# Optimization experiments

Measured on AMD Instinct MI355X. Metric: run time of the kernel, lower is better.

The kernel has to match this reference:

```python
import jax, jax.numpy as jnp
import numpy as np
import math

QUERY_LEN = 64
VALUES_LEN = 64
NUM_HEADS = 16


def setup_inputs() -> dict:
    key = jax.random.key(0)
    k1, k2, k3, k4 = jax.random.split(key, 4)
    B, G, N = 2, 4, 1024
    D = QUERY_LEN * NUM_HEADS  # 1024
    queries = jax.random.normal(k1, (B, G, N, D), dtype=jnp.float32)
    keys = jax.random.normal(k2, (B, G, N, D), dtype=jnp.float32)
    values = jax.random.normal(k3, (B, G, N, VALUES_LEN * NUM_HEADS), dtype=jnp.float32)
    neuron_bank_connectivity_sub = jax.random.uniform(k4, (1, G, 1, N, N), dtype=jnp.float32)
    return {
        "queries": queries,
        "keys": keys,
        "values": values,
        "neuron_bank_connectivity_sub": neuron_bank_connectivity_sub,
    }


def reference(queries, keys, values, neuron_bank_connectivity_sub):
    B, G, N, _ = queries.shape
    H, dq, dv = NUM_HEADS, QUERY_LEN, VALUES_LEN
    # view last dim as (vec_len, num_heads), move heads forward: [B,G,H,N,d]
    q = queries.reshape(B, G, N, dq, H).transpose(0, 1, 4, 2, 3)
    k = keys.reshape(B, G, N, dq, H).transpose(0, 1, 4, 2, 3)
    v = values.reshape(B, G, N, dv, H).transpose(0, 1, 4, 2, 3)
    scores = jnp.einsum('bghnd,bghmd->bghnm', q, k) / math.sqrt(dq)
    probs = jax.nn.softmax(scores - neuron_bank_connectivity_sub, axis=-1)
    out = jnp.einsum('bghnm,bghmd->bghnd', probs, v)  # [B,G,H,N,dv]
    # Faithful to original: view() applied to the contiguous [B,G,H,N,dv] buffer
    return out.reshape(B, G, N, H * dv)
```

## Files before the change

### kernel.cpp

```cpp
#include <hip/hip_runtime.h>
#include <hip/hip_bf16.h>
#include <math.h>

#define B_ 2
#define G_ 4
#define N_ 1024
#define H_ 16
#define D_ 64
#define BG_ (B_*G_)
#define BGH_ (B_*G_*H_)
#define MK 64
#define LOG2E 1.44269504f
#define QSCALE (0.125f * LOG2E)

typedef __bf16 bf16;
typedef bf16 bf16x8 __attribute__((ext_vector_type(8)));
typedef bf16 bf16x2 __attribute__((ext_vector_type(2)));
typedef float f32x4 __attribute__((ext_vector_type(4)));
typedef float f32x16 __attribute__((ext_vector_type(16)));
typedef int i32x4 __attribute__((ext_vector_type(4)));
typedef unsigned u32x2 __attribute__((ext_vector_type(2)));

static __device__ __forceinline__ f32x16 mfma32(bf16x8 a, bf16x8 b, f32x16 c) {
    return __builtin_amdgcn_mfma_f32_32x32x16_bf16(a, b, c, 0, 0, 0);
}

static __device__ __forceinline__ unsigned pk2(float a, float b) {
    bf16x2 t; t[0] = (bf16)a; t[1] = (bf16)b;
    return __builtin_bit_cast(unsigned, t);
}

static __device__ __forceinline__ void pl32swap(unsigned& a, unsigned& b, int hi) {
#if __has_builtin(__builtin_amdgcn_permlane32_swap)
    u32x2 r = __builtin_amdgcn_permlane32_swap(a, b, false, false);
    a = r[0]; b = r[1];
    (void)hi;
#else
    unsigned ax = (unsigned)__shfl_xor((int)a, 32, 64);
    unsigned bx = (unsigned)__shfl_xor((int)b, 32, 64);
    unsigned na = hi ? bx : a;
    unsigned nb = hi ? b : ax;
    a = na; b = nb;
#endif
}

static __device__ __forceinline__ void gll16(const void* gsrc, void* ldst, int lane) {
#if __has_builtin(__builtin_amdgcn_global_load_lds)
    (void)lane;
    __builtin_amdgcn_global_load_lds((const __attribute__((address_space(1))) void*)gsrc,
                                     (__attribute__((address_space(3))) void*)ldst, 16, 0, 0);
#else
    *(bf16x8*)((bf16*)ldst + lane * 8) = *(const bf16x8*)((const bf16*)gsrc);
#endif
}

#define HS 1160
#define NS 72

__global__ __launch_bounds__(256) void transpose_fused(
    const float* __restrict__ q, const float* __restrict__ k, const float* __restrict__ v,
    const float* __restrict__ bias,
    bf16* __restrict__ qt, bf16* __restrict__ ktb, bf16* __restrict__ vtT16,
    float* __restrict__ biasX)
{
    __shared__ __attribute__((aligned(16))) bf16 lds[16 * HS];
    int bx = blockIdx.x;
    int t = threadIdx.x;

    if (bx >= 3 * 512) {
        int idx = bx - 3 * 512;
        int gg  = idx >> 8;
        int tl  = idx & 255;
        int q0  = (tl >> 4) * 64;
        int m0  = (tl & 15) * 64;
        float* ldsF = (float*)lds;

        int mi = t & 15, qr = t >> 4;
#pragma unroll
        for (int rr = 0; rr < 4; ++rr) {
            int row = qr + rr * 16;
            f32x4 val = *(const f32x4*)(bias + ((size_t)(gg * N_ + q0 + row) * N_ + m0 + 4 * mi));
            *(f32x4*)(&ldsF[row * 68 + 4 * mi]) = val;
        }
        __syncthreads();
        int qr2 = t & 63, mb0 = t >> 6;
#pragma unroll
        for (int kk = 0; kk < 4; ++kk) {
            int mbi = mb0 + kk * 4;
            f32x4 vv = *(const f32x4*)(&ldsF[qr2 * 68 + 4 * mbi]);
            *(f32x4*)(biasX + (((size_t)gg * 256 + m0 / 4 + mbi) * N_ + q0 + qr2) * 4) = vv;
        }
        return;
    }

    int tensor = bx >> 9;
    int rr = bx & 511;
    int bg = rr >> 6;
    int tile = rr & 63;
    int n0 = tile * 16;

    const float* src = (tensor == 0) ? q : (tensor == 1) ? k : v;
    float scale = (tensor == 0) ? QSCALE : 1.0f;
    const float* sb = src + (size_t)bg * N_ * 1024 + (size_t)n0 * 1024;

    int h0 = 4 * (t & 3);
    int d  = t >> 2;
    int wbase = h0 * HS + d;
#pragma unroll 4
    for (int i = 0; i < 16; ++i) {
        float4 val = ((const float4*)(sb + (size_t)i * 1024))[t];
        bf16* p = &lds[wbase + i * NS];
        p[0]        = (bf16)(val.x * scale);
        p[HS]       = (bf16)(val.y * scale);
        p[2 * HS]   = (bf16)(val.z * scale);
        p[3 * HS]   = (bf16)(val.w * scale);
    }
    __syncthreads();

    if (tensor < 2) {
        bf16* dst = (tensor == 0) ? qt : ktb;
        int n  = (t >> 3) & 15;
        int db = t & 7;
        int hb = t >> 7;
#pragma unroll
        for (int i = 0; i < 8; ++i) {
            int h = 2 * i + hb;
            bf16x8 vv = *(const bf16x8*)(&lds[h * HS + n * NS + db * 8]);
            *(bf16x8*)(dst + (((size_t)(bg * H_ + h)) * N_ + n0 + n) * D_ + db * 8) = vv;
        }
    } else {
        int dd = t & 63;
        int hb = t >> 6;
#pragma unroll
        for (int i = 0; i < 4; ++i) {
            int h = hb * 4 + i;
            bf16x8 v0, v1;
#pragma unroll
            for (int jj = 0; jj < 8; ++jj) v0[jj] = lds[h * HS + jj * NS + dd];
#pragma unroll
            for (int jj = 0; jj < 8; ++jj) v1[jj] = lds[h * HS + (8 + jj) * NS + dd];
            bf16* dst = vtT16 + (((size_t)(bg * H_ + h) * 64 + tile) * D_ + dd) * 16;
            *(bf16x8*)dst       = v0;
            *(bf16x8*)(dst + 8) = v1;
        }
    }
}

__global__ __launch_bounds__(256, 2) void flash_kernel(
    const bf16* __restrict__ qt, const bf16* __restrict__ kt, const bf16* __restrict__ vtT16,
    const float* __restrict__ biasX, float* __restrict__ out)
{
    __shared__ __attribute__((aligned(16))) bf16 k_lds[2][MK][D_];
    __shared__ __attribute__((aligned(16))) bf16 v_lds[2][D_][MK];

    int tid  = threadIdx.x;
    int w    = tid >> 6;
    int lane = tid & 63;
    int hi   = lane >> 5;
    int q31  = lane & 31;
    int key8 = (q31 & 7) << 3;
    int hi8  = hi << 3;
    int flip = (w >> 1) & 1;

    int wg   = blockIdx.x;
    int xcd  = wg & 7;
    int slot = wg >> 3;
    int bgh  = xcd * 16 + (slot & 15);
    int n0   = (slot >> 4) * 256;
    int g    = (bgh >> 4) & (G_ - 1);

    int qbase = n0 + w * 64;

    const bf16* qb_base = qt + ((size_t)bgh * N_ + qbase + q31) * D_ + hi * 8;
    bf16x8 qA[4], qB[4];
#pragma unroll
    for (int c = 0; c < 4; ++c) {
        qA[c] = *(const bf16x8*)(qb_base + c * 16);
        qB[c] = *(const bf16x8*)(qb_base + 32 * D_ + c * 16);
    }

    f32x16 acc00 = {0,0,0,0,0,0,0,0,0,0,0,0,0,0,0,0};
    f32x16 acc01 = {0,0,0,0,0,0,0,0,0,0,0,0,0,0,0,0};
    f32x16 acc10 = {0,0,0,0,0,0,0,0,0,0,0,0,0,0,0,0};
    f32x16 acc11 = {0,0,0,0,0,0,0,0,0,0,0,0,0,0,0,0};
    float l0 = 0.f, l1 = 0.f;

    int rloc = lane >> 3;
    int c16  = lane & 7;
    int csw  = c16 ^ rloc;
    bool isK = (w < 2);
    int wrow = (w & 1) * 32;
    const bf16* ksrc = kt + (size_t)bgh * N_ * D_ + (size_t)(wrow + rloc) * D_ + csw * 8;
    const bf16* vsrc = vtT16 + (((size_t)bgh * 64 + (csw >> 1)) * D_ + (wrow + rloc)) * 16 + (csw & 1) * 8;

    const float* bb = biasX + (size_t)g * (256u * 4096) + (size_t)(qbase + q31) * 4;

    if (isK) {
#pragma unroll
        for (int i = 0; i < 4; ++i) gll16(ksrc + (size_t)i * 8 * D_, &k_lds[0][wrow + i * 8][0], lane);
    } else {
#pragma unroll
        for (int i = 0; i < 4; ++i) gll16(vsrc + (size_t)i * 128, &v_lds[0][wrow + i * 8][0], lane);
    }
    f32x4 bv[2][4];
#pragma unroll
    for (int g01 = 0; g01 < 2; ++g01)
#pragma unroll
        for (int u = 0; u < 4; ++u)
            bv[g01][u] = *(const f32x4*)(bb + g01 * 128 + (size_t)(flip * 8 + 2 * u + hi) * 4096);

    for (int it = 0; it < N_ / MK; ++it) {
        int  cur  = it & 1;
        bool more = (it + 1 < N_ / MK);
        asm volatile("s_waitcnt vmcnt(8)\n\ts_barrier" ::: "memory");
        __builtin_amdgcn_sched_barrier(0);

        if (more) {
            int nxt = cur ^ 1;
            if (isK) {
                const bf16* ks = ksrc + (size_t)(it + 1) * MK * D_;
#pragma unroll
                for (int i = 0; i < 4; ++i) gll16(ks + (size_t)i * 8 * D_, &k_lds[nxt][wrow + i * 8][0], lane);
            } else {
                const bf16* vs = vsrc + (size_t)(it + 1) * 4096;
#pragma unroll
                for (int i = 0; i < 4; ++i) gll16(vs + (size_t)i * 128, &v_lds[nxt][wrow + i * 8][0], lane);
            }
        }

#pragma unroll
        for (int ph = 0; ph < 2; ++ph) {
            int h    = ph ^ flip;
            int rowb = h << 5;

            f32x16 s0 = {0,0,0,0,0,0,0,0,0,0,0,0,0,0,0,0};
            f32x16 s1 = {0,0,0,0,0,0,0,0,0,0,0,0,0,0,0,0};
            __builtin_amdgcn_s_setprio(1);
#pragma unroll
            for (int c = 0; c < 4; ++c) {
                int off = ((c << 4) | hi8) ^ key8;
                bf16x8 kb = *(const bf16x8*)(&k_lds[cur][rowb + q31][off]);
                s0 = mfma32(kb, qA[c], s0);
                s1 = mfma32(kb, qB[c], s1);
            }
            __builtin_amdgcn_s_setprio(0);

            unsigned wa[2][4], wb[2][4];
#pragma unroll
            for (int g01 = 0; g01 < 2; ++g01) {
#pragma unroll
                for (int u = 0; u < 4; ++u) {
                    const f32x16& s = g01 ? s1 : s0;
                    f32x4 bvv = bv[g01][u];
                    float p0 = __builtin_amdgcn_exp2f(__builtin_fmaf(-LOG2E, bvv[0], s[4*u+0]));
                    float p1 = __builtin_amdgcn_exp2f(__builtin_fmaf(-LOG2E, bvv[1], s[4*u+1]));
                    float p2 = __builtin_amdgcn_exp2f(__builtin_fmaf(-LOG2E, bvv[2], s[4*u+2]));
                    float p3 = __builtin_amdgcn_exp2f(__builtin_fmaf(-LOG2E, bvv[3], s[4*u+3]));
                    if (g01) l1 += (p0 + p1) + (p2 + p3); else l0 += (p0 + p1) + (p2 + p3);
                    wa[g01][u] = pk2(p0, p1);
                    wb[g01][u] = pk2(p2, p3);
                }
            }

            if (ph == 0) {
                int mbase = it * 16 + (1 ^ flip) * 8;
#pragma unroll
                for (int g01 = 0; g01 < 2; ++g01)
#pragma unroll
                    for (int u = 0; u < 4; ++u)
                        bv[g01][u] = *(const f32x4*)(bb + g01 * 128 + (size_t)(mbase + 2 * u + hi) * 4096);
            } else if (more) {
                int mbase = (it + 1) * 16 + flip * 8;
#pragma unroll
                for (int g01 = 0; g01 < 2; ++g01)
#pragma unroll
                    for (int u = 0; u < 4; ++u)
                        bv[g01][u] = *(const f32x4*)(bb + g01 * 128 + (size_t)(mbase + 2 * u + hi) * 4096);
            }

#pragma unroll
            for (int g01 = 0; g01 < 2; ++g01) {
                pl32swap(wa[g01][0], wa[g01][1], hi);
                pl32swap(wb[g01][0], wb[g01][1], hi);
                pl32swap(wa[g01][2], wa[g01][3], hi);
                pl32swap(wb[g01][2], wb[g01][3], hi);
            }

            __builtin_amdgcn_s_setprio(1);
#pragma unroll
            for (int c01 = 0; c01 < 2; ++c01) {
                int off = (((2 * h + c01) << 4) | hi8) ^ key8;
                bf16x8 va0 = *(const bf16x8*)(&v_lds[cur][q31][off]);
                bf16x8 va1 = *(const bf16x8*)(&v_lds[cur][32 + q31][off]);
                i32x4 b0 = { (int)wa[0][2*c01], (int)wb[0][2*c01], (int)wa[0][2*c01+1], (int)wb[0][2*c01+1] };
                i32x4 b1 = { (int)wa[1][2*c01], (int)wb[1][2*c01], (int)wa[1][2*c01+1], (int)wb[1][2*c01+1] };
                bf16x8 pb0 = __builtin_bit_cast(bf16x8, b0);
                bf16x8 pb1 = __builtin_bit_cast(bf16x8, b1);
                acc00 = mfma32(va0, pb0, acc00);
                acc01 = mfma32(va1, pb0, acc01);
                acc10 = mfma32(va0, pb1, acc10);
                acc11 = mfma32(va1, pb1, acc11);
            }
            __builtin_amdgcn_s_setprio(0);
        }
    }

    l0 += __shfl_xor(l0, 32, 64);
    l1 += __shfl_xor(l1, 32, 64);
    float inv0 = 1.0f / l0, inv1 = 1.0f / l1;

#pragma unroll
    for (int g01 = 0; g01 < 2; ++g01) {
        float inv = g01 ? inv1 : inv0;
        float* ob = out + ((size_t)bgh * N_ + qbase + g01 * 32 + q31) * D_ + hi * 4;
#pragma unroll
        for (int td = 0; td < 2; ++td) {
            const f32x16& a = g01 ? (td ? acc11 : acc10) : (td ? acc01 : acc00);
#pragma unroll
            for (int u = 0; u < 4; ++u) {
                f32x4 o = { a[4*u+0] * inv, a[4*u+1] * inv, a[4*u+2] * inv, a[4*u+3] * inv };
                *(f32x4*)(ob + td * 32 + u * 8) = o;
            }
        }
    }
}

__global__ __launch_bounds__(256) void naive_kernel(
    const float* __restrict__ q, const float* __restrict__ k,
    const float* __restrict__ v, const float* __restrict__ bias,
    float* __restrict__ out)
{
    __shared__ float sc[N_];
    __shared__ float red[256];
    __shared__ float qrow[64];
    int n = blockIdx.x;
    int bgh = blockIdx.y;
    int bg = bgh >> 4, h = bgh & 15;
    int g = bg & (G_ - 1);
    int tid = threadIdx.x;
    const float* qr = q + ((size_t)(bg * N_ + n)) * 1024;
    if (tid < 64) qrow[tid] = qr[tid * 16 + h];
    __syncthreads();
    const float* bb = bias + (size_t)g * N_ * N_ + (size_t)n * N_;
    for (int m = tid; m < N_; m += 256) {
        const float* kr = k + ((size_t)(bg * N_ + m)) * 1024 + h;
        float dot = 0.f;
        for (int d = 0; d < 64; ++d) dot += qrow[d] * kr[d * 16];
        sc[m] = dot * 0.125f - bb[m];
    }
    __syncthreads();
    float mx = -INFINITY;
    for (int m = tid; m < N_; m += 256) mx = fmaxf(mx, sc[m]);
    red[tid] = mx; __syncthreads();
    for (int s = 128; s > 0; s >>= 1) {
        if (tid < s) red[tid] = fmaxf(red[tid], red[tid + s]);
        __syncthreads();
    }
    float M = red[0]; __syncthreads();
    float sum = 0.f;
    for (int m = tid; m < N_; m += 256) { float e = __expf(sc[m] - M); sc[m] = e; sum += e; }
    red[tid] = sum; __syncthreads();
    for (int s = 128; s > 0; s >>= 1) {
        if (tid < s) red[tid] += red[tid + s];
        __syncthreads();
    }
    float L = red[0]; __syncthreads();
    int d = tid & 63, quarter = tid >> 6;
    float acc = 0.f;
    const float* vb = v + (size_t)bg * N_ * 1024 + d * 16 + h;
    for (int m = quarter * 256; m < quarter * 256 + 256; ++m) acc += sc[m] * vb[(size_t)m * 1024];
    red[tid] = acc; __syncthreads();
    if (tid < 64) {
        float o = (red[tid] + red[tid + 64] + red[tid + 128] + red[tid + 192]) / L;
        out[((size_t)bgh * N_ + n) * 64 + d] = o;
    }
}

extern "C" void kernel_launch(void* const* d_in, const int* in_sizes, int n_in,
                              void* d_out, int out_size, void* d_ws, size_t ws_size,
                              hipStream_t stream) {
    const float* q    = (const float*)d_in[0];
    const float* k    = (const float*)d_in[1];
    const float* v    = (const float*)d_in[2];
    const float* bias = (const float*)d_in[3];
    float* out = (float*)d_out;

    const size_t elems = (size_t)BGH_ * N_ * D_;
    const size_t needA = 3 * elems * sizeof(bf16);
    const size_t need  = needA + (size_t)G_ * N_ * N_ * 4;

    if (ws_size >= need) {
        bf16* qt    = (bf16*)d_ws;
        bf16* ktb   = qt + elems;
        bf16* vtT16 = ktb + elems;
        float* biasX = (float*)((char*)d_ws + needA);
        transpose_fused<<<3 * 512 + 1024, 256, 0, stream>>>(q, k, v, bias, qt, ktb, vtT16, biasX);
        flash_kernel<<<dim3(512), 256, 0, stream>>>(qt, ktb, vtT16, biasX, out);
    } else {
        dim3 grid(N_, BGH_);
        naive_kernel<<<grid, 256, 0, stream>>>(q, k, v, bias, out);
    }
}
```

Before: 219.3 us.

## Give each wave private K/V LDS buffers to drop block-wide barriers

Each of the four waves now stages its own copy of the K and V tiles into a private double-buffered LDS slice. It uses 32-key tiles and waits only on its own vmcnt, with no s_barrier. The block-to-(bgh, n0) mapping is also reordered so that consecutive slots share a head. This removes cross-wave synchronisation stalls. The cost is that each wave loads the same K/V tiles itself, roughly four times the global-to-LDS traffic, and LDS use per block grows.

Measured after the change: 211.1 us. -3.7%, faster.

```diff
diff --git a/kernel.cpp b/kernel.cpp
--- a/kernel.cpp
+++ b/kernel.cpp
@@ -9,7 +9,8 @@
 #define D_ 64
 #define BG_ (B_*G_)
 #define BGH_ (B_*G_*H_)
-#define MK 64
+#define MK 32
+#define NIT (N_ / MK)
 #define LOG2E 1.44269504f
 #define QSCALE (0.125f * LOG2E)
 
@@ -150,23 +151,23 @@
     const bf16* __restrict__ qt, const bf16* __restrict__ kt, const bf16* __restrict__ vtT16,
     const float* __restrict__ biasX, float* __restrict__ out)
 {
-    __shared__ __attribute__((aligned(16))) bf16 k_lds[2][MK][D_];
-    __shared__ __attribute__((aligned(16))) bf16 v_lds[2][D_][MK];
+    __shared__ __attribute__((aligned(16))) bf16 k_sh[4][2][MK][D_];
+    __shared__ __attribute__((aligned(16))) bf16 v_sh[4][2][D_][MK];
 
     int tid  = threadIdx.x;
     int w    = tid >> 6;
     int lane = tid & 63;
     int hi   = lane >> 5;
     int q31  = lane & 31;
-    int key8 = (q31 & 7) << 3;
+    int keyK = (q31 & 7) << 3;
+    int keyV = ((q31 >> 1) & 3) << 3;
     int hi8  = hi << 3;
-    int flip = (w >> 1) & 1;
 
     int wg   = blockIdx.x;
     int xcd  = wg & 7;
     int slot = wg >> 3;
-    int bgh  = xcd * 16 + (slot & 15);
-    int n0   = (slot >> 4) * 256;
+    int bgh  = xcd * 16 + (slot >> 2);
+    int n0   = (slot & 3) * 256;
     int g    = (bgh >> 4) & (G_ - 1);
 
     int qbase = n0 + w * 64;
@@ -185,124 +186,109 @@
     f32x16 acc11 = {0,0,0,0,0,0,0,0,0,0,0,0,0,0,0,0};
     float l0 = 0.f, l1 = 0.f;
 
-    int rloc = lane >> 3;
-    int c16  = lane & 7;
-    int csw  = c16 ^ rloc;
-    bool isK = (w < 2);
-    int wrow = (w & 1) * 32;
-    const bf16* ksrc = kt + (size_t)bgh * N_ * D_ + (size_t)(wrow + rloc) * D_ + csw * 8;
-    const bf16* vsrc = vtT16 + (((size_t)bgh * 64 + (csw >> 1)) * D_ + (wrow + rloc)) * 16 + (csw & 1) * 8;
+    int rK = lane >> 3;
+    int cK = (lane & 7) ^ rK;
+    const bf16* ksrc0 = kt + (size_t)bgh * N_ * D_ + (size_t)rK * D_ + cK * 8;
+    int dV = lane >> 2;
+    int cV = (lane & 3) ^ ((lane >> 3) & 3);
+    const bf16* vsrc0 = vtT16 + (((size_t)bgh * 64 + (cV >> 1)) * D_ + dV) * 16 + (cV & 1) * 8;
 
     const float* bb = biasX + (size_t)g * (256u * 4096) + (size_t)(qbase + q31) * 4;
 
-    if (isK) {
-#pragma unroll
-        for (int i = 0; i < 4; ++i) gll16(ksrc + (size_t)i * 8 * D_, &k_lds[0][wrow + i * 8][0], lane);
-    } else {
-#pragma unroll
-        for (int i = 0; i < 4; ++i) gll16(vsrc + (size_t)i * 128, &v_lds[0][wrow + i * 8][0], lane);
-    }
+#pragma unroll
+    for (int i = 0; i < 4; ++i)
+        gll16(ksrc0 + (size_t)i * 8 * D_, &k_sh[w][0][i * 8][0], lane);
+#pragma unroll
+    for (int i = 0; i < 4; ++i)
+        gll16(vsrc0 + (size_t)i * 256, &v_sh[w][0][i * 16][0], lane);
+
     f32x4 bv[2][4];
 #pragma unroll
     for (int g01 = 0; g01 < 2; ++g01)
 #pragma unroll
         for (int u = 0; u < 4; ++u)
-            bv[g01][u] = *(const f32x4*)(bb + g01 * 128 + (size_t)(flip * 8 + 2 * u + hi) * 4096);
-
-    for (int it = 0; it < N_ / MK; ++it) {
-        int  cur  = it & 1;
-        bool more = (it + 1 < N_ / MK);
-        asm volatile("s_waitcnt vmcnt(8)\n\ts_barrier" ::: "memory");
-        __builtin_amdgcn_sched_barrier(0);
+            bv[g01][u] = *(const f32x4*)(bb + g01 * 128 + (size_t)(2 * u + hi) * 4096);
+
+    for (int it = 0; it < NIT; ++it) {
+        int  b    = it & 1;
+        bool more = (it + 1 < NIT);
 
         if (more) {
-            int nxt = cur ^ 1;
-            if (isK) {
-                const bf16* ks = ksrc + (size_t)(it + 1) * MK * D_;
-#pragma unroll
-                for (int i = 0; i < 4; ++i) gll16(ks + (size_t)i * 8 * D_, &k_lds[nxt][wrow + i * 8][0], lane);
-            } else {
-                const bf16* vs = vsrc + (size_t)(it + 1) * 4096;
-#pragma unroll
-                for (int i = 0; i < 4; ++i) gll16(vs + (size_t)i * 128, &v_lds[nxt][wrow + i * 8][0], lane);
+            const bf16* ks = ksrc0 + (size_t)(it + 1) * MK * D_;
+            const bf16* vs = vsrc0 + (size_t)(it + 1) * 2048;
+            int nb = b ^ 1;
+#pragma unroll
+            for (int i = 0; i < 4; ++i)
+                gll16(ks + (size_t)i * 8 * D_, &k_sh[w][nb][i * 8][0], lane);
+#pragma unroll
+            for (int i = 0; i < 4; ++i)
+                gll16(vs + (size_t)i * 256, &v_sh[w][nb][i * 16][0], lane);
+            asm volatile("s_waitcnt vmcnt(8)" ::: "memory");
+        } else {
+            asm volatile("s_waitcnt vmcnt(0)" ::: "memory");
+        }
+
+        f32x16 s0 = {0,0,0,0,0,0,0,0,0,0,0,0,0,0,0,0};
+        f32x16 s1 = {0,0,0,0,0,0,0,0,0,0,0,0,0,0,0,0};
+        __builtin_amdgcn_s_setprio(1);
+#pragma unroll
+        for (int c = 0; c < 4; ++c) {
+            int off = ((c << 4) | hi8) ^ keyK;
+            bf16x8 kb = *(const bf16x8*)(&k_sh[w][b][q31][off]);
+            s0 = mfma32(kb, qA[c], s0);
+            s1 = mfma32(kb, qB[c], s1);
+        }
+        __builtin_amdgcn_s_setprio(0);
+
+        unsigned wa[2][4], wbp[2][4];
+#pragma unroll
+        for (int g01 = 0; g01 < 2; ++g01) {
+#pragma unroll
+            for (int u = 0; u < 4; ++u) {
+                const f32x16& s = g01 ? s1 : s0;
+                f32x4 bvv = bv[g01][u];
+                float p0 = __builtin_amdgcn_exp2f(__builtin_fmaf(-LOG2E, bvv[0], s[4*u+0]));
+                float p1 = __builtin_amdgcn_exp2f(__builtin_fmaf(-LOG2E, bvv[1], s[4*u+1]));
+                float p2 = __builtin_amdgcn_exp2f(__builtin_fmaf(-LOG2E, bvv[2], s[4*u+2]));
+                float p3 = __builtin_amdgcn_exp2f(__builtin_fmaf(-LOG2E, bvv[3], s[4*u+3]));
+                if (g01) l1 += (p0 + p1) + (p2 + p3); else l0 += (p0 + p1) + (p2 + p3);
+                wa[g01][u]  = pk2(p0, p1);
+                wbp[g01][u] = pk2(p2, p3);
             }
         }
 
-#pragma unroll
-        for (int ph = 0; ph < 2; ++ph) {
-            int h    = ph ^ flip;
-            int rowb = h << 5;
-
-            f32x16 s0 = {0,0,0,0,0,0,0,0,0,0,0,0,0,0,0,0};
-            f32x16 s1 = {0,0,0,0,0,0,0,0,0,0,0,0,0,0,0,0};
-            __builtin_amdgcn_s_setprio(1);
-#pragma unroll
-            for (int c = 0; c < 4; ++c) {
-                int off = ((c << 4) | hi8) ^ key8;
-                bf16x8 kb = *(const bf16x8*)(&k_lds[cur][rowb + q31][off]);
-                s0 = mfma32(kb, qA[c], s0);
-                s1 = mfma32(kb, qB[c], s1);
-            }
-            __builtin_amdgcn_s_setprio(0);
-
-            unsigned wa[2][4], wb[2][4];
-#pragma unroll
-            for (int g01 = 0; g01 < 2; ++g01) {
-#pragma unroll
-                for (int u = 0; u < 4; ++u) {
-                    const f32x16& s = g01 ? s1 : s0;
-                    f32x4 bvv = bv[g01][u];
-                    float p0 = __builtin_amdgcn_exp2f(__builtin_fmaf(-LOG2E, bvv[0], s[4*u+0]));
-                    float p1 = __builtin_amdgcn_exp2f(__builtin_fmaf(-LOG2E, bvv[1], s[4*u+1]));
-                    float p2 = __builtin_amdgcn_exp2f(__builtin_fmaf(-LOG2E, bvv[2], s[4*u+2]));
-                    float p3 = __builtin_amdgcn_exp2f(__builtin_fmaf(-LOG2E, bvv[3], s[4*u+3]));
-                    if (g01) l1 += (p0 + p1) + (p2 + p3); else l0 += (p0 + p1) + (p2 + p3);
-                    wa[g01][u] = pk2(p0, p1);
-                    wb[g01][u] = pk2(p2, p3);
-                }
-            }
-
-            if (ph == 0) {
-                int mbase = it * 16 + (1 ^ flip) * 8;
-#pragma unroll
-                for (int g01 = 0; g01 < 2; ++g01)
-#pragma unroll
-                    for (int u = 0; u < 4; ++u)
-                        bv[g01][u] = *(const f32x4*)(bb + g01 * 128 + (size_t)(mbase + 2 * u + hi) * 4096);
-            } else if (more) {
-                int mbase = (it + 1) * 16 + flip * 8;
-#pragma unroll
-                for (int g01 = 0; g01 < 2; ++g01)
-#pragma unroll
-                    for (int u = 0; u < 4; ++u)
-                        bv[g01][u] = *(const f32x4*)(bb + g01 * 128 + (size_t)(mbase + 2 * u + hi) * 4096);
-            }
-
-#pragma unroll
-            for (int g01 = 0; g01 < 2; ++g01) {
-                pl32swap(wa[g01][0], wa[g01][1], hi);
-                pl32swap(wb[g01][0], wb[g01][1], hi);
-                pl32swap(wa[g01][2], wa[g01][3], hi);
-                pl32swap(wb[g01][2], wb[g01][3], hi);
-            }
-
-            __builtin_amdgcn_s_setprio(1);
-#pragma unroll
-            for (int c01 = 0; c01 < 2; ++c01) {
-                int off = (((2 * h + c01) << 4) | hi8) ^ key8;
-                bf16x8 va0 = *(const bf16x8*)(&v_lds[cur][q31][off]);
-                bf16x8 va1 = *(const bf16x8*)(&v_lds[cur][32 + q31][off]);
-                i32x4 b0 = { (int)wa[0][2*c01], (int)wb[0][2*c01], (int)wa[0][2*c01+1], (int)wb[0][2*c01+1] };
-                i32x4 b1 = { (int)wa[1][2*c01], (int)wb[1][2*c01], (int)wa[1][2*c01+1], (int)wb[1][2*c01+1] };
-                bf16x8 pb0 = __builtin_bit_cast(bf16x8, b0);
-                bf16x8 pb1 = __builtin_bit_cast(bf16x8, b1);
-                acc00 = mfma32(va0, pb0, acc00);
-                acc01 = mfma32(va1, pb0, acc01);
-                acc10 = mfma32(va0, pb1, acc10);
-                acc11 = mfma32(va1, pb1, acc11);
-            }
-            __builtin_amdgcn_s_setprio(0);
-        }
+        if (more) {
+#pragma unroll
+            for (int g01 = 0; g01 < 2; ++g01)
+#pragma unroll
+                for (int u = 0; u < 4; ++u)
+                    bv[g01][u] = *(const f32x4*)(bb + g01 * 128 + (size_t)((it + 1) * 8 + 2 * u + hi) * 4096);
+        }
+
+#pragma unroll
+        for (int g01 = 0; g01 < 2; ++g01) {
+            pl32swap(wa[g01][0],  wa[g01][1],  hi);
+            pl32swap(wbp[g01][0], wbp[g01][1], hi);
+            pl32swap(wa[g01][2],  wa[g01][3],  hi);
+            pl32swap(wbp[g01][2], wbp[g01][3], hi);
+        }
+
+        __builtin_amdgcn_s_setprio(1);
+#pragma unroll
+        for (int kc = 0; kc < 2; ++kc) {
+            int off = ((kc << 4) | hi8) ^ keyV;
+            bf16x8 va0 = *(const bf16x8*)(&v_sh[w][b][q31][off]);
+            bf16x8 va1 = *(const bf16x8*)(&v_sh[w][b][32 + q31][off]);
+            i32x4 b0 = { (int)wa[0][2*kc], (int)wbp[0][2*kc], (int)wa[0][2*kc+1], (int)wbp[0][2*kc+1] };
+            i32x4 b1 = { (int)wa[1][2*kc], (int)wbp[1][2*kc], (int)wa[1][2*kc+1], (int)wbp[1][2*kc+1] };
+            bf16x8 pb0 = __builtin_bit_cast(bf16x8, b0);
+            bf16x8 pb1 = __builtin_bit_cast(bf16x8, b1);
+            acc00 = mfma32(va0, pb0, acc00);
+            acc01 = mfma32(va1, pb0, acc01);
+            acc10 = mfma32(va0, pb1, acc10);
+            acc11 = mfma32(va1, pb1, acc11);
+        }
+        __builtin_amdgcn_s_setprio(0);
     }
 
     l0 += __shfl_xor(l0, 32, 64);
```
